# Kernel tuning notes

Hardware: AMD Instinct MI355X
Metric: run time of the kernel (lower is better)

The kernel has to match this reference:

```python
import jax, jax.numpy as jnp
import numpy as np

N_USERS = 10000
RESERVE = 100
N_TOTAL = N_USERS + RESERVE  # 10100 graph nodes (incl. unknown-user slots)
D = 128                      # user_id_embedding_size
B = 2048                     # batch of user ids
AVG_DEG = 32


def _build_friendship_matrix(rng: np.random.Generator) -> np.ndarray:
    # Dense symmetric friendship matrix with 1.0 on the diagonal (self-loop),
    # mirroring torch.diag(ones) + symmetric weighted edge insertion.
    F = np.zeros((N_TOTAL, N_TOTAL), dtype=np.float32)
    np.fill_diagonal(F, 1.0)
    n_edges = N_USERS * AVG_DEG // 2
    src = rng.integers(0, N_USERS, size=n_edges)
    dst = rng.integers(0, N_USERS, size=n_edges)
    w = rng.uniform(0.1, 1.0, size=n_edges).astype(np.float32)
    F[src, dst] = w
    F[dst, src] = w
    return F


def setup_inputs() -> dict:
    key = jax.random.key(0)
    k_ids, k_emb, k_w, k_b = jax.random.split(key, 4)
    rng = np.random.default_rng(0)
    user_ids = jax.random.randint(k_ids, (B,), 0, N_USERS, dtype=jnp.int32)
    friendship_matrix = jnp.asarray(_build_friendship_matrix(rng))      # (N, N)
    # torch init: embeddings ~ U[0,1); Linear weight/bias ~ U[-1/sqrt(d), 1/sqrt(d)]
    user_id_embeddings = jax.random.uniform(k_emb, (N_TOTAL, D), dtype=jnp.float32)
    bound = 1.0 / np.sqrt(D)
    lin_weight = jax.random.uniform(k_w, (D, D), minval=-bound, maxval=bound, dtype=jnp.float32)
    lin_bias = jax.random.uniform(k_b, (D,), minval=-bound, maxval=bound, dtype=jnp.float32)
    return {
        "user_ids": user_ids,
        "friendship_matrix": friendship_matrix,
        "user_id_embeddings": user_id_embeddings,
        "lin_weight": lin_weight,
        "lin_bias": lin_bias,
    }


def reference(user_ids, friendship_matrix, user_id_embeddings, lin_weight, lin_bias):
    # Per user: friends = F[uid]; aggregated = sum_n friends[n] * E[n]
    # Vectorized over the batch: gather rows of F, then one GEMM with E.
    friends = friendship_matrix[user_ids]                 # (B, N)
    aggregated = friends @ user_id_embeddings             # (B, D)
    # torch.nn.Linear: x @ W^T + b
    return aggregated @ lin_weight.T + lin_bias           # (B, D)
```

## Files before the change

### kernel.cpp

```cpp
#include <hip/hip_runtime.h>


#define NTOT 10100
#define NV4  2525
#define DIM  128
#define TPB  256
#define RPW  10
#define WCAP 64

__global__ __launch_bounds__(TPB) void friendship_kernel(
    const int*   __restrict__ uids,
    const float* __restrict__ F,
    const float* __restrict__ E,
    const float* __restrict__ W,
    const float* __restrict__ bias,
    float*       __restrict__ out)
{
    __shared__ int    s_n[4][WCAP];
    __shared__ float4 s_v[4][WCAP];
    __shared__ float  s_part[4][DIM];
    __shared__ float  s_agg[DIM];
    __shared__ float  s_out[DIM];

    const int row  = blockIdx.x;
    const int tid  = threadIdx.x;
    const int w    = tid >> 6;
    const int lane = tid & 63;
    const int uid  = uids[row];
    const float* Frow = F + (size_t)uid * NTOT;
    const float4* Frow4 = (const float4*)Frow;
    const unsigned long long below = (1ULL << lane) - 1ULL;

    int  cb  = 0;
    bool ovf = false;
    #pragma unroll
    for (int t = 0; t < RPW; ++t) {
        const int j = 640 * w + 64 * t + lane;
        float4 v = make_float4(0.f, 0.f, 0.f, 0.f);
        if (j < NV4) v = Frow4[j];
        const bool nz = (v.x != 0.0f) | (v.y != 0.0f) | (v.z != 0.0f) | (v.w != 0.0f);
        const unsigned long long m = __ballot(nz);
        if (m) {
            const int cnt = __popcll(m);
            if (cb + cnt <= WCAP) {
                const int p = cb + __popcll(m & below);
                if (nz) { s_n[w][p] = j; s_v[w][p] = v; }
                cb += cnt;
            } else {
                ovf = true;
            }
        }
    }
    asm volatile("s_waitcnt lgkmcnt(0)" ::: "memory");
    __builtin_amdgcn_sched_barrier(0);

    float2 acc = make_float2(0.0f, 0.0f);
    const float* Ed = E + 2 * lane;
    if (!ovf) {
        for (int k = 0; k < cb; ++k) {
            const int    j4 = s_n[w][k];
            const float4 v  = s_v[w][k];
            const int n = j4 * 4;
            if (v.x != 0.0f) { float2 e = *(const float2*)(Ed + (size_t)(n    ) * DIM); acc.x += v.x * e.x; acc.y += v.x * e.y; }
            if (v.y != 0.0f) { float2 e = *(const float2*)(Ed + (size_t)(n + 1) * DIM); acc.x += v.y * e.x; acc.y += v.y * e.y; }
            if (v.z != 0.0f) { float2 e = *(const float2*)(Ed + (size_t)(n + 2) * DIM); acc.x += v.z * e.x; acc.y += v.z * e.y; }
            if (v.w != 0.0f) { float2 e = *(const float2*)(Ed + (size_t)(n + 3) * DIM); acc.x += v.w * e.x; acc.y += v.w * e.y; }
        }
    } else {
        const int nbeg = 2560 * w;
        const int nend = (2560 * (w + 1) < NTOT) ? 2560 * (w + 1) : NTOT;
        for (int n = nbeg; n < nend; ++n) {
            float fw = Frow[n];
            if (fw != 0.0f) {
                float2 e = *(const float2*)(Ed + (size_t)n * DIM);
                acc.x += fw * e.x; acc.y += fw * e.y;
            }
        }
    }
    *(float2*)&s_part[w][2 * lane] = acc;
    __syncthreads();

    if (tid < DIM)
        s_agg[tid] = s_part[0][tid] + s_part[1][tid] + s_part[2][tid] + s_part[3][tid];
    __syncthreads();

    const float4* W4 = (const float4*)W;
    #pragma unroll
    for (int q = 0; q < 16; ++q) {
        int i4 = tid + TPB * q;
        float4 wv = W4[i4];
        int j  = i4 >> 5;
        int dd = (i4 & 31) * 4;
        float4 ag = *(const float4*)&s_agg[dd];
        float p = wv.x * ag.x + wv.y * ag.y + wv.z * ag.z + wv.w * ag.w;
        p += __shfl_xor(p, 16);
        p += __shfl_xor(p, 8);
        p += __shfl_xor(p, 4);
        p += __shfl_xor(p, 2);
        p += __shfl_xor(p, 1);
        if ((tid & 31) == 0) s_out[j] = p;
    }
    __syncthreads();
    if (tid < DIM)
        out[(size_t)row * DIM + tid] = bias[tid] + s_out[tid];
}

extern "C" void kernel_launch(void* const* d_in, const int* in_sizes, int n_in,
                              void* d_out, int out_size, void* d_ws, size_t ws_size,
                              hipStream_t stream) {
    const int*   uids = (const int*)  d_in[0];
    const float* F    = (const float*)d_in[1];
    const float* E    = (const float*)d_in[2];
    const float* W    = (const float*)d_in[3];
    const float* bias = (const float*)d_in[4];
    float*       out  = (float*)d_out;

    const int B = in_sizes[0];
    friendship_kernel<<<B, TPB, 0, stream>>>(uids, F, E, W, bias, out);
}
```

Baseline: 32.77 us.

## Split row scan and aggregation into two kernels via workspace compaction

The fused kernel becomes two launches. The first scans each gathered friendship row and writes the compacted nonzero float4 indices and values, plus per-wave counts, to a global workspace. The second reads those lists to gather embeddings and apply the linear layer. Rebalancing the per-wave chunk size and lowering the list cap is meant to separate the bandwidth-bound scan from the latency-bound gather and let each run at its own occupancy. The cost is an extra launch and a workspace round trip through global memory, and the smaller cap makes the slow dense fallback more likely.

```diff
diff --git a/kernel.cpp b/kernel.cpp
--- a/kernel.cpp
+++ b/kernel.cpp
@@ -5,61 +5,82 @@
 #define NV4  2525
 #define DIM  128
 #define TPB  256
-#define RPW  10
-#define WCAP 64
+#define NW   4
+#define QV4  632
+#define WC   40
 
-__global__ __launch_bounds__(TPB) void friendship_kernel(
+__global__ __launch_bounds__(TPB) void scan_kernel(
     const int*   __restrict__ uids,
     const float* __restrict__ F,
-    const float* __restrict__ E,
-    const float* __restrict__ W,
-    const float* __restrict__ bias,
-    float*       __restrict__ out)
+    int*         __restrict__ g_cnt,
+    int*         __restrict__ g_idx,
+    float4*      __restrict__ g_val)
 {
-    __shared__ int    s_n[4][WCAP];
-    __shared__ float4 s_v[4][WCAP];
-    __shared__ float  s_part[4][DIM];
-    __shared__ float  s_agg[DIM];
-    __shared__ float  s_out[DIM];
+    const int row  = blockIdx.x;
+    const int tid  = threadIdx.x;
+    const int w    = tid >> 6;
+    const int lane = tid & 63;
+    const float4* Frow4 = (const float4*)(F + (size_t)uids[row] * NTOT);
+    const unsigned long long below = (1ULL << lane) - 1ULL;
+
+    const int jbeg = w * QV4;
+    const int jend = (w == 3) ? NV4 : (jbeg + QV4);
+    int*    my_idx = g_idx + ((size_t)row * NW + w) * WC;
+    float4* my_val = g_val + ((size_t)row * NW + w) * WC;
+
+    int  cb  = 0;
+    bool ovf = false;
+    #pragma unroll
+    for (int t = 0; t < 10; ++t) {
+        const int j = jbeg + t * 64 + lane;
+        float4 v = make_float4(0.f, 0.f, 0.f, 0.f);
+        if (t < 9)          v = Frow4[j];
+        else if (j < jend)  v = Frow4[j];
+        const bool nz = (v.x != 0.0f) | (v.y != 0.0f) | (v.z != 0.0f) | (v.w != 0.0f);
+        const unsigned long long m = __ballot(nz);
+        if (m) {
+            const int c = __popcll(m);
+            if (cb + c <= WC) {
+                const int p = cb + __popcll(m & below);
+                if (nz) { my_idx[p] = j; my_val[p] = v; }
+                cb += c;
+            } else {
+                ovf = true;
+            }
+        }
+    }
+    if (lane == 0) g_cnt[row * NW + w] = ovf ? -1 : cb;
+}
+
+__global__ __launch_bounds__(TPB) void agg_lin_kernel(
+    const int*    __restrict__ uids,
+    const float*  __restrict__ F,
+    const float*  __restrict__ E,
+    const float*  __restrict__ W,
+    const float*  __restrict__ bias,
+    const int*    __restrict__ g_cnt,
+    const int*    __restrict__ g_idx,
+    const float4* __restrict__ g_val,
+    float*        __restrict__ out)
+{
+    __shared__ float s_part[NW][DIM];
+    __shared__ float s_agg[DIM];
+    __shared__ float s_out[DIM];
 
     const int row  = blockIdx.x;
     const int tid  = threadIdx.x;
     const int w    = tid >> 6;
     const int lane = tid & 63;
-    const int uid  = uids[row];
-    const float* Frow = F + (size_t)uid * NTOT;
-    const float4* Frow4 = (const float4*)Frow;
-    const unsigned long long below = (1ULL << lane) - 1ULL;
-
-    int  cb  = 0;
-    bool ovf = false;
-    #pragma unroll
-    for (int t = 0; t < RPW; ++t) {
-        const int j = 640 * w + 64 * t + lane;
-        float4 v = make_float4(0.f, 0.f, 0.f, 0.f);
-        if (j < NV4) v = Frow4[j];
-        const bool nz = (v.x != 0.0f) | (v.y != 0.0f) | (v.z != 0.0f) | (v.w != 0.0f);
-        const unsigned long long m = __ballot(nz);
-        if (m) {
-            const int cnt = __popcll(m);
-            if (cb + cnt <= WCAP) {
-                const int p = cb + __popcll(m & below);
-                if (nz) { s_n[w][p] = j; s_v[w][p] = v; }
-                cb += cnt;
-            } else {
-                ovf = true;
-            }
-        }
-    }
-    asm volatile("s_waitcnt lgkmcnt(0)" ::: "memory");
-    __builtin_amdgcn_sched_barrier(0);
+    const int cnt  = g_cnt[row * NW + w];
+    const int*    my_idx = g_idx + ((size_t)row * NW + w) * WC;
+    const float4* my_val = g_val + ((size_t)row * NW + w) * WC;
+    const float* Ed = E + 2 * lane;
 
     float2 acc = make_float2(0.0f, 0.0f);
-    const float* Ed = E + 2 * lane;
-    if (!ovf) {
-        for (int k = 0; k < cb; ++k) {
-            const int    j4 = s_n[w][k];
-            const float4 v  = s_v[w][k];
+    if (cnt >= 0) {
+        for (int k = 0; k < cnt; ++k) {
+            const int    j4 = my_idx[k];
+            const float4 v  = my_val[k];
             const int n = j4 * 4;
             if (v.x != 0.0f) { float2 e = *(const float2*)(Ed + (size_t)(n    ) * DIM); acc.x += v.x * e.x; acc.y += v.x * e.y; }
             if (v.y != 0.0f) { float2 e = *(const float2*)(Ed + (size_t)(n + 1) * DIM); acc.x += v.y * e.x; acc.y += v.y * e.y; }
@@ -67,8 +88,9 @@
             if (v.w != 0.0f) { float2 e = *(const float2*)(Ed + (size_t)(n + 3) * DIM); acc.x += v.w * e.x; acc.y += v.w * e.y; }
         }
     } else {
-        const int nbeg = 2560 * w;
-        const int nend = (2560 * (w + 1) < NTOT) ? 2560 * (w + 1) : NTOT;
+        const float* Frow = F + (size_t)uids[row] * NTOT;
+        const int nbeg = w * QV4 * 4;
+        const int nend = (w == 3) ? NTOT : ((w + 1) * QV4 * 4);
         for (int n = nbeg; n < nend; ++n) {
             float fw = Frow[n];
             if (fw != 0.0f) {
@@ -116,5 +138,11 @@
     float*       out  = (float*)d_out;
 
     const int B = in_sizes[0];
-    friendship_kernel<<<B, TPB, 0, stream>>>(uids, F, E, W, bias, out);
+    char* ws = (char*)d_ws;
+    float4* g_val = (float4*)ws;
+    int*    g_idx = (int*)(ws + (size_t)B * NW * WC * 16);
+    int*    g_cnt = (int*)(ws + (size_t)B * NW * WC * 20);
+
+    scan_kernel<<<B, TPB, 0, stream>>>(uids, F, g_cnt, g_idx, g_val);
+    agg_lin_kernel<<<B, TPB, 0, stream>>>(uids, F, E, W, bias, g_cnt, g_idx, g_val, out);
 }
```

Result: slower. 38.40 us (+17.2%).
